# Kernel tuning notes

Measured on AMD Instinct MI355X. Metric: run time of the kernel, lower is better.

Reference implementation:

```python
import jax, jax.numpy as jnp
import numpy as np

N_ORDERS = 2
CHUNK = 64            # real tokens per chunk
LINEAR_ACTIVATION = False
STAB = 10000.0


def _ensure_stability(x):
    x = jnp.clip(x, -STAB, STAB)
    return jnp.nan_to_num(x, nan=0.0, posinf=STAB, neginf=-STAB)


def setup_inputs() -> dict:
    key = jax.random.key(0)
    k1, k2, k3, k4 = jax.random.split(key, 4)
    B, H, NC, D = 2, 16, 32, 128
    CT = CHUNK * N_ORDERS  # 128 virtual tokens per chunk
    s = 1.0 / np.sqrt(D)
    q_chunks = jax.random.normal(k1, (B, H, NC, CT, D), jnp.float32) * s
    W = jax.random.normal(k2, (B, H, NC, CT, D), jnp.float32) * s
    U = jax.random.normal(k3, (B, H, NC, CT, D), jnp.float32) * s
    h0 = jax.random.normal(k4, (B, H, D, D), jnp.float32) * s
    return {"q_chunks": q_chunks, "W": W, "U": U, "h0": h0}


def _gelu_norm(h):
    # h_norm/2 * gelu(2*h/h_norm, tanh) applied to chunk-boundary state
    n = jnp.linalg.norm(h, axis=-1, keepdims=True) + 1e-6
    return n / 2.0 * jax.nn.gelu(2.0 * h / n, approximate=True)


def _delta_product_scan(q_chunks, W, U, h0):
    B, H, NC, CT, D = q_chunks.shape
    C = CT // N_ORDERS

    def body(h, chunk):
        q_c, w_c, u_c = chunk  # each [B,H,CT,D]
        # virtual-token layout: token c, step s lives at index c*n_orders+s
        qs = q_c.reshape(B, H, C, N_ORDERS, D)
        ws = w_c.reshape(B, H, C, N_ORDERS, D)
        us = u_c.reshape(B, H, C, N_ORDERS, D)
        state = jnp.broadcast_to(h[:, :, None], (B, H, C, D, D))  # per-token state
        outs = []
        for step in range(N_ORDERS):
            q_s = qs[:, :, :, step]
            w_s = ws[:, :, :, step]
            u_s = us[:, :, :, step]
            k_trans_h = jnp.einsum('bhcd,bhcde->bhce', w_s, state)
            u_val = u_s - k_trans_h
            o_inter = jnp.einsum('bhcd,bhcde->bhce', q_s, state)
            o_intra = q_s * u_val  # elementwise, as in source
            outs.append(o_intra + o_inter)
            state = _ensure_stability(state + w_s[..., :, None] * u_val[..., None, :])
        out = jnp.stack(outs, axis=3).reshape(B, H, CT, D)
        h_new = state[:, :, -1]
        if not LINEAR_ACTIVATION:
            h_new = _gelu_norm(h_new)
        return h_new, out

    chunks = (jnp.moveaxis(q_chunks, 2, 0), jnp.moveaxis(W, 2, 0), jnp.moveaxis(U, 2, 0))
    h_final, ys = jax.lax.scan(body, h0, chunks)
    return jnp.moveaxis(ys, 0, 2), h_final  # [B,H,NC,CT,D], [B,H,D,D]


def reference(q_chunks, W, U, h0):
    return _delta_product_scan(q_chunks, W, U, h0)
```

## Files before the change

kernel.cpp:

```cpp
#include <hip/hip_runtime.h>


#define Dd 128
#define NCH 32
#define YS 16777216

typedef __attribute__((ext_vector_type(4))) float floatx4;
typedef __attribute__((ext_vector_type(8))) short short8;

__device__ __forceinline__ unsigned cvtpk(float lo, float hi) {
  unsigned r;
  asm("v_cvt_pk_bf16_f32 %0, %1, %2" : "=v"(r) : "v"(lo), "v"(hi));
  return r;
}

#define ROTADD(p, CTRL)                                              \
  p += __uint_as_float((unsigned)__builtin_amdgcn_update_dpp(        \
      0, (int)__float_as_uint(p), (CTRL), 0xF, 0xF, false))

__global__ __launch_bounds__(512) void p1_scan(const float* __restrict__ W,
    const float* __restrict__ U, const float* __restrict__ h0,
    unsigned short* __restrict__ hws, float* __restrict__ out) {
  __shared__ float wpre[NCH * 320];
  __shared__ float upre[NCH * 2 * Dd];
  __shared__ float d10pre[NCH];
  __shared__ float sqb[Dd * 129];
  __shared__ float ppart[8 * 132];
  __shared__ float nrm2[4 * 40];

  const int bh = blockIdx.x;
  const int t = threadIdx.x;
  const int w = t >> 6, l = t & 63;
  const int cl = l & 15;
  const int c = (w << 4) | cl;
  const int rg = l >> 4;

  {
    const float* Wg = W + (size_t)bh * NCH * 16384;
    const float* Ug = U + (size_t)bh * NCH * 16384;
#pragma unroll
    for (int k = 0; k < 4; k++) {
      int idx4 = k * 512 + t;
      int n = idx4 >> 6;
      int rem = idx4 & 63;
      int r = rem >> 5, e4 = (rem & 31) * 4;
      size_t g = (size_t)n * 16384 + (size_t)(126 + r) * Dd + e4;
      *(float4*)&upre[idx4 * 4] = *(const float4*)&Ug[g];
      *(float4*)&wpre[n * 320 + r * 160 + (e4 >> 5) * 40 + (e4 & 31)] =
          *(const float4*)&Wg[g];
    }
  }
  {
    const float4* hg = (const float4*)(h0 + (size_t)bh * 16384);
#pragma unroll
    for (int k = 0; k < 8; k++) {
      int idx4 = k * 512 + t;
      float4 v = hg[idx4];
      int d = idx4 >> 5, e4 = (idx4 & 31) * 4;
      sqb[d * 129 + e4 + 0] = v.x;
      sqb[d * 129 + e4 + 1] = v.y;
      sqb[d * 129 + e4 + 2] = v.z;
      sqb[d * 129 + e4 + 3] = v.w;
    }
  }
  __syncthreads();
  {
    int n = t >> 4, j = t & 15;
    const float* w0p = &wpre[n * 320 + (j >> 2) * 40 + (j & 3) * 8];
    const float* w1p = w0p + 160;
    float p = 0.f;
#pragma unroll
    for (int i = 0; i < 8; i++) p += w0p[i] * w1p[i];
    p += __shfl_xor(p, 1, 64);
    p += __shfl_xor(p, 2, 64);
    p += __shfl_xor(p, 4, 64);
    p += __shfl_xor(p, 8, 64);
    if (j == 0) d10pre[n] = p;
  }
  float hr[32];
#pragma unroll
  for (int i = 0; i < 32; i++) hr[i] = sqb[(rg * 32 + i) * 129 + c];
  __syncthreads();

  unsigned short* hwsb = hws + (size_t)bh * NCH * 16384;
  {
    unsigned pk[16];
#pragma unroll
    for (int i = 0; i < 16; i++) pk[i] = cvtpk(hr[2 * i], hr[2 * i + 1]);
    uint4* dst = (uint4*)(hwsb + (size_t)c * Dd + rg * 32);
    dst[0] = make_uint4(pk[0], pk[1], pk[2], pk[3]);
    dst[1] = make_uint4(pk[4], pk[5], pk[6], pk[7]);
    dst[2] = make_uint4(pk[8], pk[9], pk[10], pk[11]);
    dst[3] = make_uint4(pk[12], pk[13], pk[14], pk[15]);
  }

  for (int n = 0; n < NCH; n++) {
    floatx4 w0v[8], w1v[8];
    const float* wb = &wpre[n * 320 + rg * 40];
#pragma unroll
    for (int i = 0; i < 8; i++) {
      w0v[i] = *(const floatx4*)&wb[4 * i];
      w1v[i] = *(const floatx4*)&wb[160 + 4 * i];
    }
    float a0 = 0.f, a1 = 0.f, b0 = 0.f, b1 = 0.f;
#pragma unroll
    for (int i = 0; i < 8; i += 2) {
#pragma unroll
      for (int j = 0; j < 4; j++) {
        float h0v = hr[4 * i + j];
        float h1v = hr[4 * i + 4 + j];
        a0 = fmaf(w0v[i][j], h0v, a0);
        a1 = fmaf(w1v[i][j], h0v, a1);
        b0 = fmaf(w0v[i + 1][j], h1v, b0);
        b1 = fmaf(w1v[i + 1][j], h1v, b1);
      }
    }
    a0 += b0; a1 += b1;
    a0 += __shfl_xor(a0, 16, 64);
    a0 += __shfl_xor(a0, 32, 64);
    a1 += __shfl_xor(a1, 16, 64);
    a1 += __shfl_xor(a1, 32, 64);
    const float u0 = upre[n * 256 + c];
    const float u1 = upre[n * 256 + Dd + c];
    const float d10 = d10pre[n];
    const float uv0 = u0 - a0;
    const float uv1 = u1 - a1 - d10 * uv0;
#pragma unroll
    for (int i = 0; i < 8; i++)
#pragma unroll
      for (int j = 0; j < 4; j++) {
        int ii = 4 * i + j;
        float s = __builtin_amdgcn_fmed3f(fmaf(w0v[i][j], uv0, hr[ii]),
                                          -10000.0f, 10000.0f);
        s = __builtin_amdgcn_fmed3f(fmaf(w1v[i][j], uv1, s),
                                    -10000.0f, 10000.0f);
        hr[ii] = s;
      }
    {
      float r0s = 0.f, r1s = 0.f;
#pragma unroll
      for (int i = 0; i < 32; i++) {
        float p = hr[i] * hr[i];
        ROTADD(p, 0x128);
        ROTADD(p, 0x124);
        ROTADD(p, 0x122);
        ROTADD(p, 0x121);
        if (i < 16) r0s = (cl == i) ? p : r0s;
        else        r1s = (cl == i - 16) ? p : r1s;
      }
      float* ppw = &ppart[w * 132 + rg * 32];
      ppw[(cl + 13 * rg) & 31] = r0s;
      ppw[(cl + 16 + 13 * rg) & 31] = r1s;
    }
    __syncthreads();
    if (t < 128) {
      int rgq = t >> 5, rr = t & 31;
      int slot = rgq * 32 + ((rr + 13 * rgq) & 31);
      float s = (ppart[slot] + ppart[132 + slot]) +
                (ppart[264 + slot] + ppart[396 + slot]) +
                (ppart[528 + slot] + ppart[660 + slot]) +
                (ppart[792 + slot] + ppart[924 + slot]);
      float nd = sqrtf(s) + 1e-6f;
      nrm2[rgq * 40 + rr] = __fdividef(2.0f, nd);
    }
    __syncthreads();
    floatx4 r2v[8];
    const float* nb = &nrm2[rg * 40];
#pragma unroll
    for (int i = 0; i < 8; i++) r2v[i] = *(const floatx4*)&nb[4 * i];
#pragma unroll
    for (int i = 0; i < 8; i++)
#pragma unroll
      for (int j = 0; j < 4; j++) {
        int ii = 4 * i + j;
        float h = hr[ii];
        float x = h * r2v[i][j];
        float x2 = x * x;
        float aa = x * fmaf(0.071354816f, x2, 1.59576912f);
        float ex = __expf(-aa);
        hr[ii] = __fdividef(h, 1.0f + ex);
      }
    if (n < NCH - 1) {
      unsigned pk[16];
#pragma unroll
      for (int i = 0; i < 16; i++) pk[i] = cvtpk(hr[2 * i], hr[2 * i + 1]);
      uint4* dst = (uint4*)(hwsb + (size_t)(n + 1) * 16384 + (size_t)c * Dd + rg * 32);
      dst[0] = make_uint4(pk[0], pk[1], pk[2], pk[3]);
      dst[1] = make_uint4(pk[4], pk[5], pk[6], pk[7]);
      dst[2] = make_uint4(pk[8], pk[9], pk[10], pk[11]);
      dst[3] = make_uint4(pk[12], pk[13], pk[14], pk[15]);
    } else {
      float* ob = out + YS + (size_t)bh * 16384;
#pragma unroll
      for (int i = 0; i < 32; i++) ob[(rg * 32 + i) * Dd + c] = hr[i];
    }
  }
}


__device__ __forceinline__ void stage_slice(const float* Qb, const float* Wb,
    float* qd, float* wd, int kc, int wv6, int ln) {
#pragma unroll
  for (int i = 0; i < 4; i++) {
    int cb = i * 512 + wv6 * 64;
    int isW = cb >> 10;
    int cbm = cb & 1023;
    int c = cbm + ln;
    int r = c >> 3;
    int s = (c >> 4) & 7;
    const float* g = (isW ? Wb : Qb) + r * Dd + kc * 32 + (((c & 7) ^ s) << 2);
    float* l = (isW ? wd : qd) + (cbm << 2);
    __builtin_amdgcn_global_load_lds(
        (const __attribute__((address_space(1))) void*)g,
        (__attribute__((address_space(3))) void*)l, 16, 0, 0);
  }
}

__global__ __launch_bounds__(512, 4) void p2_out(const float* __restrict__ Q,
    const float* __restrict__ W, const float* __restrict__ U,
    const unsigned short* __restrict__ hws, float* __restrict__ out) {
  __shared__ unsigned short hT[Dd * 136];
  __shared__ float qsl[4096];
  __shared__ float wsl[4096];
  __shared__ float d10s[64], dq1s[64];
  __shared__ float dps[512];

  const int bid = blockIdx.x;
  const int n = bid & 31, bh = bid >> 5;
  const size_t base = (size_t)(bh * NCH + n) * 16384;
  const float* Qb = Q + base;
  const float* Wb = W + base;
  const float* Ub = U + base;
  float* Ob = out + base;
  const int t = threadIdx.x;
  const int wv6 = t >> 6, ln = t & 63;

  stage_slice(Qb, Wb, &qsl[0], &wsl[0], 0, wv6, ln);

  {
    const uint4* src = (const uint4*)(hws + base);
#pragma unroll
    for (int i = 0; i < 4; i++) {
      int idx = t + i * 512;
      uint4 v = src[idx];
      int e = idx >> 4, j = idx & 15;
      *(uint4*)&hT[e * 136 + j * 8] = v;
    }
  }
  {
    int which = t >> 8, tt = t & 255;
    int cc = tt >> 2, part = tt & 3;
    const float4* ar = (const float4*)((which ? Qb : Wb) + (2 * cc + 1) * Dd + part * 32);
    const float4* w0r = (const float4*)(Wb + (2 * cc) * Dd + part * 32);
    float s = 0.f;
#pragma unroll
    for (int i = 0; i < 8; i++) {
      float4 a = ar[i], b = w0r[i];
      s += a.x * b.x + a.y * b.y + a.z * b.z + a.w * b.w;
    }
    dps[which * 256 + tt] = s;
  }
  __syncthreads();
  if (t < 128) {
    int which = t >> 6, cc = t & 63;
    const float* p = dps + which * 256 + cc * 4;
    float s = p[0] + p[1] + p[2] + p[3];
    (which ? dq1s : d10s)[cc] = s;
  }

  const int pr = wv6 >> 2, eq = wv6 & 3;
  const int lm = ln & 15, lq = ln >> 4;
  const int sw = lm & 7;
  const int i0 = ((2 * lq) ^ sw) << 2;
  const int i1 = ((2 * lq + 1) ^ sw) << 2;

  floatx4 acc[2][4][2];
#pragma unroll
  for (int m = 0; m < 2; m++)
#pragma unroll
    for (int ci = 0; ci < 4; ci++)
#pragma unroll
      for (int j = 0; j < 2; j++) acc[m][ci][j] = (floatx4){0.f, 0.f, 0.f, 0.f};

  for (int kc = 0; kc < 4; kc++) {
    const int k0 = kc * 32;
    short8 bfr[2];
#pragma unroll
    for (int j = 0; j < 2; j++) {
      int ee = (2 * eq + j) * 16 + lm;
      bfr[j] = *(const short8*)&hT[ee * 136 + k0 + 8 * lq];
    }
#pragma unroll
    for (int ci = 0; ci < 4; ci++) {
      const int rb = (32 * ci + 2 * lm) * 32 + pr * 32;
      {
        const float* p = &qsl[rb];
        floatx4 g0 = *(const floatx4*)(p + i0);
        floatx4 g1 = *(const floatx4*)(p + i1);
        union { short8 v; unsigned u[4]; } af;
        af.u[0] = cvtpk(g0[0], g0[1]);
        af.u[1] = cvtpk(g0[2], g0[3]);
        af.u[2] = cvtpk(g1[0], g1[1]);
        af.u[3] = cvtpk(g1[2], g1[3]);
        acc[0][ci][0] = __builtin_amdgcn_mfma_f32_16x16x32_bf16(af.v, bfr[0], acc[0][ci][0], 0, 0, 0);
        acc[0][ci][1] = __builtin_amdgcn_mfma_f32_16x16x32_bf16(af.v, bfr[1], acc[0][ci][1], 0, 0, 0);
      }
      {
        const float* p = &wsl[rb];
        floatx4 g0 = *(const floatx4*)(p + i0);
        floatx4 g1 = *(const floatx4*)(p + i1);
        union { short8 v; unsigned u[4]; } af;
        af.u[0] = cvtpk(g0[0], g0[1]);
        af.u[1] = cvtpk(g0[2], g0[3]);
        af.u[2] = cvtpk(g1[0], g1[1]);
        af.u[3] = cvtpk(g1[2], g1[3]);
        acc[1][ci][0] = __builtin_amdgcn_mfma_f32_16x16x32_bf16(af.v, bfr[0], acc[1][ci][0], 0, 0, 0);
        acc[1][ci][1] = __builtin_amdgcn_mfma_f32_16x16x32_bf16(af.v, bfr[1], acc[1][ci][1], 0, 0, 0);
      }
    }
    __syncthreads();
    if (kc < 3) {
      stage_slice(Qb, Wb, &qsl[0], &wsl[0], kc + 1, wv6, ln);
      __syncthreads();
    }
  }

  float* uv0s = (float*)hT;
  if (pr == 0) {
#pragma unroll
    for (int ci = 0; ci < 4; ci++)
#pragma unroll
      for (int j = 0; j < 2; j++) {
        int ee = (2 * eq + j) * 16 + lm;
#pragma unroll
        for (int r = 0; r < 4; r++) {
          int cc = ci * 16 + lq * 4 + r;
          float T0 = acc[1][ci][j][r];
          float Q0h = acc[0][ci][j][r];
          float u0 = Ub[(2 * cc) * Dd + ee];
          float q0 = Qb[(2 * cc) * Dd + ee];
          float uv0 = u0 - T0;
          uv0s[cc * Dd + ee] = uv0;
          Ob[(2 * cc) * Dd + ee] = q0 * uv0 + Q0h;
        }
      }
  }
  __syncthreads();
  if (pr == 1) {
#pragma unroll
    for (int ci = 0; ci < 4; ci++)
#pragma unroll
      for (int j = 0; j < 2; j++) {
        int ee = (2 * eq + j) * 16 + lm;
#pragma unroll
        for (int r = 0; r < 4; r++) {
          int cc = ci * 16 + lq * 4 + r;
          float T1 = acc[1][ci][j][r];
          float Q1h = acc[0][ci][j][r];
          float u1 = Ub[(2 * cc + 1) * Dd + ee];
          float q1 = Qb[(2 * cc + 1) * Dd + ee];
          float uv0 = uv0s[cc * Dd + ee];
          float uv1 = u1 - T1 - d10s[cc] * uv0;
          Ob[(2 * cc + 1) * Dd + ee] = q1 * uv1 + Q1h + dq1s[cc] * uv0;
        }
      }
  }
}

extern "C" void kernel_launch(void* const* d_in, const int* in_sizes, int n_in,
                              void* d_out, int out_size, void* d_ws, size_t ws_size,
                              hipStream_t stream) {
  const float* Q = (const float*)d_in[0];
  const float* W = (const float*)d_in[1];
  const float* U = (const float*)d_in[2];
  const float* h0 = (const float*)d_in[3];
  float* out = (float*)d_out;
  unsigned short* hws = (unsigned short*)d_ws;

  p1_scan<<<32, 512, 0, stream>>>(W, U, h0, hws, out);
  p2_out<<<1024, 512, 0, stream>>>(Q, W, U, hws, out);
}
```

Before: 394.1 us.

## Double scan block to 1024 threads and compute row norms via shared memory

The serial scan kernel p1_scan now runs 1024 threads per block instead of 512, so each thread holds 16 state elements instead of 32. The per-row norm is now computed by writing the updated state into shared memory (with a rotated column layout) and reducing along rows, replacing the DPP rotate-add plus partial-sum pass. This shortens the per-chunk serial critical path on a latency-bound kernel that only launches 32 blocks. In exchange it adds more shuffle-reduction steps, extra shared-memory stores with a possible bank-conflict risk, and more barrier cost with twice as many waves.

```diff
diff --git a/kernel.cpp b/kernel.cpp
--- a/kernel.cpp
+++ b/kernel.cpp
@@ -14,47 +14,42 @@
   return r;
 }
 
-#define ROTADD(p, CTRL)                                              \
-  p += __uint_as_float((unsigned)__builtin_amdgcn_update_dpp(        \
-      0, (int)__float_as_uint(p), (CTRL), 0xF, 0xF, false))
-
-__global__ __launch_bounds__(512) void p1_scan(const float* __restrict__ W,
+__global__ __launch_bounds__(1024, 4) void p1_scan(const float* __restrict__ W,
     const float* __restrict__ U, const float* __restrict__ h0,
     unsigned short* __restrict__ hws, float* __restrict__ out) {
   __shared__ float wpre[NCH * 320];
   __shared__ float upre[NCH * 2 * Dd];
   __shared__ float d10pre[NCH];
   __shared__ float sqb[Dd * 129];
-  __shared__ float ppart[8 * 132];
-  __shared__ float nrm2[4 * 40];
+  __shared__ float nrm2[8 * 20];
 
   const int bh = blockIdx.x;
   const int t = threadIdx.x;
   const int w = t >> 6, l = t & 63;
-  const int cl = l & 15;
-  const int c = (w << 4) | cl;
-  const int rg = l >> 4;
+  const int cl = l & 7;
+  const int c = (w << 3) | cl;
+  const int rg = l >> 3;
 
   {
     const float* Wg = W + (size_t)bh * NCH * 16384;
     const float* Ug = U + (size_t)bh * NCH * 16384;
 #pragma unroll
-    for (int k = 0; k < 4; k++) {
-      int idx4 = k * 512 + t;
+    for (int k = 0; k < 2; k++) {
+      int idx4 = k * 1024 + t;
       int n = idx4 >> 6;
       int rem = idx4 & 63;
       int r = rem >> 5, e4 = (rem & 31) * 4;
       size_t g = (size_t)n * 16384 + (size_t)(126 + r) * Dd + e4;
       *(float4*)&upre[idx4 * 4] = *(const float4*)&Ug[g];
-      *(float4*)&wpre[n * 320 + r * 160 + (e4 >> 5) * 40 + (e4 & 31)] =
+      *(float4*)&wpre[n * 320 + r * 160 + (e4 >> 4) * 20 + (e4 & 15)] =
           *(const float4*)&Wg[g];
     }
   }
   {
     const float4* hg = (const float4*)(h0 + (size_t)bh * 16384);
 #pragma unroll
-    for (int k = 0; k < 8; k++) {
-      int idx4 = k * 512 + t;
+    for (int k = 0; k < 4; k++) {
+      int idx4 = k * 1024 + t;
       float4 v = hg[idx4];
       int d = idx4 >> 5, e4 = (idx4 & 31) * 4;
       sqb[d * 129 + e4 + 0] = v.x;
@@ -65,46 +60,50 @@
   }
   __syncthreads();
   {
-    int n = t >> 4, j = t & 15;
-    const float* w0p = &wpre[n * 320 + (j >> 2) * 40 + (j & 3) * 8];
+    int n = t >> 5, j = t & 31;
+    const float* w0p = &wpre[n * 320 + (j >> 2) * 20 + (j & 3) * 4];
     const float* w1p = w0p + 160;
     float p = 0.f;
 #pragma unroll
-    for (int i = 0; i < 8; i++) p += w0p[i] * w1p[i];
+    for (int i = 0; i < 4; i++) p += w0p[i] * w1p[i];
     p += __shfl_xor(p, 1, 64);
     p += __shfl_xor(p, 2, 64);
     p += __shfl_xor(p, 4, 64);
     p += __shfl_xor(p, 8, 64);
+    p += __shfl_xor(p, 16, 64);
     if (j == 0) d10pre[n] = p;
   }
-  float hr[32];
-#pragma unroll
-  for (int i = 0; i < 32; i++) hr[i] = sqb[(rg * 32 + i) * 129 + c];
+  float hr[16];
+#pragma unroll
+  for (int i = 0; i < 16; i++) hr[i] = sqb[(rg * 16 + i) * 129 + c];
   __syncthreads();
 
+  const int cpos = (c & 96) | ((c + 20 * rg) & 31);
+  float* sqw = &sqb[rg * 16 * 129 + cpos];
+  const int srow = t >> 3, sst = t & 7;
+  const float* sqr = &sqb[srow * 129 + sst * 16];
+
   unsigned short* hwsb = hws + (size_t)bh * NCH * 16384;
   {
-    unsigned pk[16];
-#pragma unroll
-    for (int i = 0; i < 16; i++) pk[i] = cvtpk(hr[2 * i], hr[2 * i + 1]);
-    uint4* dst = (uint4*)(hwsb + (size_t)c * Dd + rg * 32);
+    unsigned pk[8];
+#pragma unroll
+    for (int i = 0; i < 8; i++) pk[i] = cvtpk(hr[2 * i], hr[2 * i + 1]);
+    uint4* dst = (uint4*)(hwsb + (size_t)c * Dd + rg * 16);
     dst[0] = make_uint4(pk[0], pk[1], pk[2], pk[3]);
     dst[1] = make_uint4(pk[4], pk[5], pk[6], pk[7]);
-    dst[2] = make_uint4(pk[8], pk[9], pk[10], pk[11]);
-    dst[3] = make_uint4(pk[12], pk[13], pk[14], pk[15]);
   }
 
   for (int n = 0; n < NCH; n++) {
-    floatx4 w0v[8], w1v[8];
-    const float* wb = &wpre[n * 320 + rg * 40];
-#pragma unroll
-    for (int i = 0; i < 8; i++) {
+    floatx4 w0v[4], w1v[4];
+    const float* wb = &wpre[n * 320 + rg * 20];
+#pragma unroll
+    for (int i = 0; i < 4; i++) {
       w0v[i] = *(const floatx4*)&wb[4 * i];
       w1v[i] = *(const floatx4*)&wb[160 + 4 * i];
     }
     float a0 = 0.f, a1 = 0.f, b0 = 0.f, b1 = 0.f;
 #pragma unroll
-    for (int i = 0; i < 8; i += 2) {
+    for (int i = 0; i < 4; i += 2) {
 #pragma unroll
       for (int j = 0; j < 4; j++) {
         float h0v = hr[4 * i + j];
@@ -116,8 +115,10 @@
       }
     }
     a0 += b0; a1 += b1;
+    a0 += __shfl_xor(a0, 8, 64);
     a0 += __shfl_xor(a0, 16, 64);
     a0 += __shfl_xor(a0, 32, 64);
+    a1 += __shfl_xor(a1, 8, 64);
     a1 += __shfl_xor(a1, 16, 64);
     a1 += __shfl_xor(a1, 32, 64);
     const float u0 = upre[n * 256 + c];
@@ -126,7 +127,7 @@
     const float uv0 = u0 - a0;
     const float uv1 = u1 - a1 - d10 * uv0;
 #pragma unroll
-    for (int i = 0; i < 8; i++)
+    for (int i = 0; i < 4; i++)
 #pragma unroll
       for (int j = 0; j < 4; j++) {
         int ii = 4 * i + j;
@@ -135,41 +136,36 @@
         s = __builtin_amdgcn_fmed3f(fmaf(w1v[i][j], uv1, s),
                                     -10000.0f, 10000.0f);
         hr[ii] = s;
-      }
+        sqw[ii * 129] = s;
+      }
+    __syncthreads();
     {
-      float r0s = 0.f, r1s = 0.f;
-#pragma unroll
-      for (int i = 0; i < 32; i++) {
-        float p = hr[i] * hr[i];
-        ROTADD(p, 0x128);
-        ROTADD(p, 0x124);
-        ROTADD(p, 0x122);
-        ROTADD(p, 0x121);
-        if (i < 16) r0s = (cl == i) ? p : r0s;
-        else        r1s = (cl == i - 16) ? p : r1s;
-      }
-      float* ppw = &ppart[w * 132 + rg * 32];
-      ppw[(cl + 13 * rg) & 31] = r0s;
-      ppw[(cl + 16 + 13 * rg) & 31] = r1s;
+      float acc = 0.f, acc2 = 0.f;
+#pragma unroll
+      for (int b = 0; b < 4; b++) {
+        const float* p = sqr + 4 * ((b + sst) & 3);
+        float v0 = p[0], v1 = p[1], v2 = p[2], v3 = p[3];
+        acc = fmaf(v0, v0, acc);
+        acc2 = fmaf(v1, v1, acc2);
+        acc = fmaf(v2, v2, acc);
+        acc2 = fmaf(v3, v3, acc2);
+      }
+      acc += acc2;
+      acc += __shfl_xor(acc, 1, 64);
+      acc += __shfl_xor(acc, 2, 64);
+      acc += __shfl_xor(acc, 4, 64);
+      if (sst == 0) {
+        float nd = sqrtf(acc) + 1e-6f;
+        nrm2[(srow >> 4) * 20 + (srow & 15)] = __fdividef(2.0f, nd);
+      }
     }
     __syncthreads();
-    if (t < 128) {
-      int rgq = t >> 5, rr = t & 31;
-      int slot = rgq * 32 + ((rr + 13 * rgq) & 31);
-      float s = (ppart[slot] + ppart[132 + slot]) +
-                (ppart[264 + slot] + ppart[396 + slot]) +
-                (ppart[528 + slot] + ppart[660 + slot]) +
-                (ppart[792 + slot] + ppart[924 + slot]);
-      float nd = sqrtf(s) + 1e-6f;
-      nrm2[rgq * 40 + rr] = __fdividef(2.0f, nd);
-    }
-    __syncthreads();
-    floatx4 r2v[8];
-    const float* nb = &nrm2[rg * 40];
-#pragma unroll
-    for (int i = 0; i < 8; i++) r2v[i] = *(const floatx4*)&nb[4 * i];
-#pragma unroll
-    for (int i = 0; i < 8; i++)
+    floatx4 r2v[4];
+    const float* nb = &nrm2[rg * 20];
+#pragma unroll
+    for (int i = 0; i < 4; i++) r2v[i] = *(const floatx4*)&nb[4 * i];
+#pragma unroll
+    for (int i = 0; i < 4; i++)
 #pragma unroll
       for (int j = 0; j < 4; j++) {
         int ii = 4 * i + j;
@@ -181,18 +177,16 @@
         hr[ii] = __fdividef(h, 1.0f + ex);
       }
     if (n < NCH - 1) {
-      unsigned pk[16];
-#pragma unroll
-      for (int i = 0; i < 16; i++) pk[i] = cvtpk(hr[2 * i], hr[2 * i + 1]);
-      uint4* dst = (uint4*)(hwsb + (size_t)(n + 1) * 16384 + (size_t)c * Dd + rg * 32);
+      unsigned pk[8];
+#pragma unroll
+      for (int i = 0; i < 8; i++) pk[i] = cvtpk(hr[2 * i], hr[2 * i + 1]);
+      uint4* dst = (uint4*)(hwsb + (size_t)(n + 1) * 16384 + (size_t)c * Dd + rg * 16);
       dst[0] = make_uint4(pk[0], pk[1], pk[2], pk[3]);
       dst[1] = make_uint4(pk[4], pk[5], pk[6], pk[7]);
-      dst[2] = make_uint4(pk[8], pk[9], pk[10], pk[11]);
-      dst[3] = make_uint4(pk[12], pk[13], pk[14], pk[15]);
     } else {
       float* ob = out + YS + (size_t)bh * 16384;
 #pragma unroll
-      for (int i = 0; i < 32; i++) ob[(rg * 32 + i) * Dd + c] = hr[i];
+      for (int i = 0; i < 16; i++) ob[(rg * 16 + i) * Dd + c] = hr[i];
     }
   }
 }
@@ -377,6 +371,6 @@
   float* out = (float*)d_out;
   unsigned short* hws = (unsigned short*)d_ws;
 
-  p1_scan<<<32, 512, 0, stream>>>(W, U, h0, hws, out);
+  p1_scan<<<32, 1024, 0, stream>>>(W, U, h0, hws, out);
   p2_out<<<1024, 512, 0, stream>>>(Q, W, U, hws, out);
 }
```

Measured after the change: 375.7 us. 1.05x faster.
